# Performance work log

Measured on AMD Instinct MI355X. Metric: run time of the kernel, lower is better.

Reference implementation:

```python
import jax, jax.numpy as jnp
import numpy as np

DIM = 2048
N_HEADS = 16
HEAD_DIM = DIM // N_HEADS
ROPE_BASE = 10000


def l2norm(x, axis=-1, eps=1e-12):
    n = jnp.sqrt(jnp.sum(x * x, axis=axis, keepdims=True))
    return x / jnp.maximum(n, eps)


def rope_tables(T, dim, base, dtype):
    theta = 1.0 / (base ** (jnp.arange(0, dim, 2, dtype=dtype) / dim))  # [dim/2]
    ang = jnp.arange(T, dtype=dtype)[:, None] * theta[None, :]          # [T, dim/2]
    return jnp.sin(ang), jnp.cos(ang)


def apply_rope(x, sin, cos):
    # x: [B, H, T, D]; sin/cos: [T, D/2] (half-split convention, not interleaved)
    half = x.shape[-1] // 2
    xr, xi = x[..., :half], x[..., half:]
    yr = xr * cos - xi * sin
    yi = xr * sin + xi * cos
    return jnp.concatenate([yr, yi], axis=-1)


def setup_inputs() -> dict:
    key = jax.random.key(0)
    ks = jax.random.split(key, 5)
    B, T = 1, 2048
    x = jax.random.normal(ks[0], (B, T, DIM), dtype=jnp.float32)
    wq = jax.random.normal(ks[1], (DIM, DIM), dtype=jnp.float32) * 0.02
    wk = jax.random.normal(ks[2], (DIM, DIM), dtype=jnp.float32) * 0.02
    wv = jax.random.normal(ks[3], (DIM, DIM), dtype=jnp.float32) * 0.02
    wo = jax.random.normal(ks[4], (DIM, DIM), dtype=jnp.float32) * 0.02
    sqk = jnp.ones((N_HEADS, 1, HEAD_DIM), dtype=jnp.float32) * (1.0 / DIM ** 0.5)
    return {"x": x, "wq": wq, "wk": wk, "wv": wv, "wo": wo, "sqk": sqk}


def reference(x, wq, wk, wv, wo, sqk):
    B, T, C = x.shape
    H, D = N_HEADS, HEAD_DIM
    restore = C ** 0.5  # restore_scale_sqk = sqkinit / sqkscale
    actual_sqk = sqk * restore  # [H, 1, D]

    def proj(w):
        return jnp.einsum('btc,oc->bto', x, w).reshape(B, T, H, D).transpose(0, 2, 1, 3)

    q = proj(wq)  # [B, H, T, D]
    new_k = proj(wk)
    new_v = proj(wv)

    sin, cos = rope_tables(T, D, ROPE_BASE, x.dtype)
    q = apply_rope(q, sin, cos) * actual_sqk
    k = apply_rope(new_k, sin, cos) * actual_sqk

    # NOTE: original uses scale=head_dim**0.5 (multiplies by sqrt(D))
    scores = jnp.einsum('bhqd,bhkd->bhqk', q, k) * (D ** 0.5)
    mask = jnp.tril(jnp.ones((T, T), dtype=bool))
    scores = jnp.where(mask, scores, jnp.finfo(scores.dtype).min)
    attn = jax.nn.softmax(scores, axis=-1)
    out = jnp.einsum('bhqk,bhkd->bhqd', attn, new_v)  # [B, H, T, D]
    out = out.transpose(0, 2, 1, 3).reshape(B, T, C)
    out = jnp.einsum('btc,oc->bto', out, wo)
    return (l2norm(out), (new_k, new_v))
```

## Files before the change

kernel.cpp:

```cpp
#include <hip/hip_runtime.h>

typedef __bf16 bf16x8 __attribute__((ext_vector_type(8)));
typedef float f32x4 __attribute__((ext_vector_type(4)));
typedef unsigned short us4 __attribute__((ext_vector_type(4)));

constexpr int TT = 2048;
constexpr int CC = 2048;
constexpr int HH = 16;
constexpr int DD = 128;

__device__ __forceinline__ unsigned short f2bf(float f) {
  unsigned u = __builtin_bit_cast(unsigned, f);
  u += 0x7FFFu + ((u >> 16) & 1u);
  return (unsigned short)(u >> 16);
}
__device__ __forceinline__ float bf2f(unsigned short b) {
  unsigned u = ((unsigned)b) << 16;
  return __builtin_bit_cast(float, u);
}

__device__ __forceinline__ void gld_lds16(const unsigned short* g, unsigned short* l) {
  __builtin_amdgcn_global_load_lds(
      (const __attribute__((address_space(1))) unsigned int*)g,
      (__attribute__((address_space(3))) unsigned int*)l,
      16, 0, 0);
}

__global__ __launch_bounds__(256) void k_cvt5(
    const float* __restrict__ s0, const float* __restrict__ s1,
    const float* __restrict__ s2, const float* __restrict__ s3,
    const float* __restrict__ s4,
    unsigned short* __restrict__ d0, unsigned short* __restrict__ d1,
    unsigned short* __restrict__ d2, unsigned short* __restrict__ d3,
    unsigned short* __restrict__ d4) {
  const int m = blockIdx.y;
  const float* src = (m == 0) ? s0 : (m == 1) ? s1 : (m == 2) ? s2 : (m == 3) ? s3 : s4;
  unsigned short* dst = (m == 0) ? d0 : (m == 1) ? d1 : (m == 2) ? d2 : (m == 3) ? d3 : d4;
  int i = blockIdx.x * 256 + threadIdx.x;
  const float4* s = (const float4*)src;
  float4 a = s[2 * i], b = s[2 * i + 1];
  us4 lo = { f2bf(a.x), f2bf(a.y), f2bf(a.z), f2bf(a.w) };
  us4 hi = { f2bf(b.x), f2bf(b.y), f2bf(b.z), f2bf(b.w) };
  us4* d = (us4*)dst;
  d[2 * i] = lo;
  d[2 * i + 1] = hi;
}

#define WAIT_LGKM0                                      \
  asm volatile("s_waitcnt lgkmcnt(0)" ::: "memory");    \
  __builtin_amdgcn_sched_barrier(0);
#define BAR __builtin_amdgcn_s_barrier();

__global__ __launch_bounds__(512, 2) void k_gemm192(
    const unsigned short* __restrict__ A, const unsigned short* __restrict__ B,
    unsigned short* __restrict__ qraw,
    float* __restrict__ outk, float* __restrict__ outv,
    unsigned short* __restrict__ vtb) {
  __shared__ alignas(16) unsigned short As[2][256 * 64];
  __shared__ alignas(16) unsigned short Bs[2][192 * 64];
  const int K = CC, NT = K >> 6, NT2 = NT >> 1;
  const int tid = threadIdx.x;
  const int m0 = blockIdx.y * 256, n0 = blockIdx.x * 192;
  const int wid = tid >> 6, lane = tid & 63;
  const int wr = wid >> 2, wc = wid & 3;
  const int lr = lane & 15, lg = lane >> 4;

  auto stA = [&](int buf, int jb, int tile) {
#pragma unroll
    for (int j = jb; j < jb + 2; ++j) {
      const int ch = tid + j * 512;
      const int r = ch >> 3, c8 = ch & 7;
      gld_lds16(A + (size_t)(m0 + r) * K + tile * 64 + ((c8 ^ (r & 7)) * 8),
                &As[buf][ch * 8]);
    }
  };
  auto stB2 = [&](int buf, int tile) {
#pragma unroll
    for (int j = 0; j < 2; ++j) {
      const int ch = tid + j * 512;
      const int r = ch >> 3, c8 = ch & 7;
      gld_lds16(B + (size_t)(n0 + r) * K + tile * 64 + ((c8 ^ (r & 7)) * 8),
                &Bs[buf][ch * 8]);
    }
  };
  auto stB1 = [&](int buf, int tile) {
    const int ch = tid + 1024;
    const int r = ch >> 3, c8 = ch & 7;
    gld_lds16(B + (size_t)(n0 + r) * K + tile * 64 + ((c8 ^ (r & 7)) * 8),
              &Bs[buf][ch * 8]);
  };

  f32x4 acc[8][3] = {};
  bf16x8 alo[4][2], ahi[4][2], b01[2][2], b2v[2];

  auto rdAlo = [&](int d) {
#pragma unroll
    for (int im = 0; im < 4; ++im)
#pragma unroll
      for (int kk = 0; kk < 2; ++kk) {
        const int row = wr * 128 + im * 16 + lr;
        alo[im][kk] = *(const bf16x8*)(&As[d][row * 64 + (((kk * 4 + lg) ^ (row & 7)) * 8)]);
      }
  };
  auto rdAhi = [&](int d) {
#pragma unroll
    for (int im = 0; im < 4; ++im)
#pragma unroll
      for (int kk = 0; kk < 2; ++kk) {
        const int row = wr * 128 + (4 + im) * 16 + lr;
        ahi[im][kk] = *(const bf16x8*)(&As[d][row * 64 + (((kk * 4 + lg) ^ (row & 7)) * 8)]);
      }
  };
  auto rdB01 = [&](int d) {
#pragma unroll
    for (int in = 0; in < 2; ++in)
#pragma unroll
      for (int kk = 0; kk < 2; ++kk) {
        const int row = wc * 48 + in * 16 + lr;
        b01[in][kk] = *(const bf16x8*)(&Bs[d][row * 64 + (((kk * 4 + lg) ^ (row & 7)) * 8)]);
      }
  };
  auto rdB2 = [&](int d) {
#pragma unroll
    for (int kk = 0; kk < 2; ++kk) {
      const int row = wc * 48 + 32 + lr;
      b2v[kk] = *(const bf16x8*)(&Bs[d][row * 64 + (((kk * 4 + lg) ^ (row & 7)) * 8)]);
    }
  };

  auto q_lo01 = [&]() {
    __builtin_amdgcn_s_setprio(1);
#pragma unroll
    for (int im = 0; im < 4; ++im)
#pragma unroll
      for (int in = 0; in < 2; ++in)
#pragma unroll
        for (int kk = 0; kk < 2; ++kk)
          acc[im][in] = __builtin_amdgcn_mfma_f32_16x16x32_bf16(alo[im][kk], b01[in][kk], acc[im][in], 0, 0, 0);
    __builtin_amdgcn_s_setprio(0);
  };
  auto q_mid16 = [&]() {
    __builtin_amdgcn_s_setprio(1);
#pragma unroll
    for (int im = 0; im < 4; ++im)
#pragma unroll
      for (int kk = 0; kk < 2; ++kk)
        acc[im][2] = __builtin_amdgcn_mfma_f32_16x16x32_bf16(alo[im][kk], b2v[kk], acc[im][2], 0, 0, 0);
#pragma unroll
    for (int im = 0; im < 4; ++im)
#pragma unroll
      for (int kk = 0; kk < 2; ++kk)
        acc[4 + im][2] = __builtin_amdgcn_mfma_f32_16x16x32_bf16(ahi[im][kk], b2v[kk], acc[4 + im][2], 0, 0, 0);
    __builtin_amdgcn_s_setprio(0);
  };
  auto q_hi01 = [&]() {
    __builtin_amdgcn_s_setprio(1);
#pragma unroll
    for (int im = 0; im < 4; ++im)
#pragma unroll
      for (int in = 0; in < 2; ++in)
#pragma unroll
        for (int kk = 0; kk < 2; ++kk)
          acc[4 + im][in] = __builtin_amdgcn_mfma_f32_16x16x32_bf16(ahi[im][kk], b01[in][kk], acc[4 + im][in], 0, 0, 0);
    __builtin_amdgcn_s_setprio(0);
  };

  stB2(0, 0); stB1(0, 0); stA(0, 0, 0); stA(0, 2, 0);
  stB2(1, 1); stB1(1, 1);
  asm volatile("s_waitcnt vmcnt(3)" ::: "memory");
  __builtin_amdgcn_sched_barrier(0);
  BAR

  for (int t = 0; t < NT2; ++t) {
    const int t1 = 2 * t + 1, t2 = 2 * t + 2, t3 = 2 * t + 3;
    const bool s2 = t2 < NT;

    rdAlo(0); rdB01(0);
    stA(1, 0, t1);
    BAR WAIT_LGKM0
    q_lo01();
    BAR
    rdB2(0); rdAhi(0);
    stA(1, 2, t1);
    BAR WAIT_LGKM0
    q_mid16();
    BAR
    if (s2) { stB2(0, t2); stB1(0, t2); }
    q_hi01();
    if (s2) { asm volatile("s_waitcnt vmcnt(3)" ::: "memory"); }
    else    { asm volatile("s_waitcnt vmcnt(0)" ::: "memory"); }
    __builtin_amdgcn_sched_barrier(0);
    BAR

    rdAlo(1); rdB01(1);
    if (s2) stA(0, 0, t2);
    BAR WAIT_LGKM0
    q_lo01();
    BAR
    rdB2(1); rdAhi(1);
    if (s2) stA(0, 2, t2);
    BAR WAIT_LGKM0
    q_mid16();
    BAR
    if (s2) { stB2(1, t3); stB1(1, t3); }
    q_hi01();
    if (s2) { asm volatile("s_waitcnt vmcnt(3)" ::: "memory"); }
    else    { asm volatile("s_waitcnt vmcnt(0)" ::: "memory"); }
    __builtin_amdgcn_sched_barrier(0);
    BAR
  }

#pragma unroll
  for (int mf = 0; mf < 8; ++mf) {
    const int row = m0 + wr * 128 + mf * 16 + lg * 4;
#pragma unroll
    for (int nf = 0; nf < 3; ++nf) {
      const int col = n0 + wc * 48 + nf * 16 + lr;
      if (col < 2048) {
#pragma unroll
        for (int r = 0; r < 4; ++r)
          qraw[(size_t)(row + r) * 2048 + col] = f2bf(acc[mf][nf][r]);
      } else if (col < 4096) {
        const int c = col - 2048;
#pragma unroll
        for (int r = 0; r < 4; ++r)
          outk[(size_t)(c >> 7) * (TT * DD) + (size_t)(row + r) * DD + (c & 127)] = acc[mf][nf][r];
      } else {
        const int c = col - 4096;
        const int hh = c >> 7, d2 = c & 127;
        us4 tv;
#pragma unroll
        for (int r = 0; r < 4; ++r) {
          float v = acc[mf][nf][r];
          outv[(size_t)hh * (TT * DD) + (size_t)(row + r) * DD + d2] = v;
          tv[r] = f2bf(v);
        }
        *(us4*)(vtb + (size_t)hh * (size_t)(DD * TT) + (size_t)d2 * TT + row) = tv;
      }
    }
  }
}

__global__ __launch_bounds__(512, 2) void k_gemm8p(
    const unsigned short* __restrict__ A, const unsigned short* __restrict__ B,
    int N, int K, int kspan,
    unsigned short* __restrict__ out0, unsigned short* __restrict__ out1,
    unsigned short* __restrict__ out2, unsigned short* __restrict__ out3) {
  __shared__ alignas(16) unsigned short As[2][2][128 * 64];
  __shared__ alignas(16) unsigned short Bs[2][2][128 * 64];
  const int tid = threadIdx.x;
  const int m0 = blockIdx.y * 256, n0 = blockIdx.x * 256;
  const int kbeg = blockIdx.z * kspan;
  const int NT = kspan >> 6, NT2 = NT >> 1;
  const int wid = tid >> 6, lane = tid & 63;
  const int wr = wid >> 2, wc = wid & 3;
  const int lr = lane & 15, lg = lane >> 4;
  const int bh = wc >> 1, brow0 = (wc & 1) * 64;

  const int sr0 = tid >> 3, sc0 = tid & 7;
  const unsigned short* Ab = A + kbeg;
  const unsigned short* Bb = B + kbeg;

  auto stageA = [&](int buf, int half, int tile) {
    const int koff = tile * 64;
#pragma unroll
    for (int j = 0; j < 2; ++j) {
      const int r = sr0 + j * 64;
      gld_lds16(Ab + (size_t)(m0 + half * 128 + r) * K + koff + ((sc0 ^ (r & 7)) * 8),
                &As[buf][half][(tid + j * 512) * 8]);
    }
  };
  auto stageB = [&](int buf, int half, int tile) {
    const int koff = tile * 64;
#pragma unroll
    for (int j = 0; j < 2; ++j) {
      const int r = sr0 + j * 64;
      gld_lds16(Bb + (size_t)(n0 + half * 128 + r) * K + koff + ((sc0 ^ (r & 7)) * 8),
                &Bs[buf][half][(tid + j * 512) * 8]);
    }
  };

  f32x4 acc[8][4] = {};
  bf16x8 alo[4][2], ahi[4][2], ba[2][2], bb[2][2];

  auto rdAlo = [&](int d) {
#pragma unroll
    for (int im = 0; im < 4; ++im)
#pragma unroll
      for (int kk = 0; kk < 2; ++kk) {
        const int row = im * 16 + lr;
        alo[im][kk] = *(const bf16x8*)(&As[d][wr][row * 64 + (((kk * 4 + lg) ^ (row & 7)) * 8)]);
      }
  };
  auto rdAhi = [&](int d) {
#pragma unroll
    for (int im = 0; im < 4; ++im)
#pragma unroll
      for (int kk = 0; kk < 2; ++kk) {
        const int row = (4 + im) * 16 + lr;
        ahi[im][kk] = *(const bf16x8*)(&As[d][wr][row * 64 + (((kk * 4 + lg) ^ (row & 7)) * 8)]);
      }
  };
  auto rdBa = [&](int d) {
#pragma unroll
    for (int in = 0; in < 2; ++in)
#pragma unroll
      for (int kk = 0; kk < 2; ++kk) {
        const int row = brow0 + in * 16 + lr;
        ba[in][kk] = *(const bf16x8*)(&Bs[d][bh][row * 64 + (((kk * 4 + lg) ^ (row & 7)) * 8)]);
      }
  };
  auto rdBb = [&](int d) {
#pragma unroll
    for (int in = 0; in < 2; ++in)
#pragma unroll
      for (int kk = 0; kk < 2; ++kk) {
        const int row = brow0 + (2 + in) * 16 + lr;
        bb[in][kk] = *(const bf16x8*)(&Bs[d][bh][row * 64 + (((kk * 4 + lg) ^ (row & 7)) * 8)]);
      }
  };

#define MFMA_Q(MB, NB, AF, BF)                                                     \
  _Pragma("unroll") for (int im = 0; im < 4; ++im)                                 \
      _Pragma("unroll") for (int in = 0; in < 2; ++in)                             \
          _Pragma("unroll") for (int kk = 0; kk < 2; ++kk)                         \
              acc[MB + im][NB + in] = __builtin_amdgcn_mfma_f32_16x16x32_bf16(     \
                  AF[im][kk], BF[in][kk], acc[MB + im][NB + in], 0, 0, 0);

  stageB(0, 0, 0); stageB(0, 1, 0); stageA(0, 0, 0); stageA(0, 1, 0);
  if (NT > 1) { stageB(1, 0, 1); stageB(1, 1, 1); }
  asm volatile("s_waitcnt vmcnt(4)" ::: "memory");
  __builtin_amdgcn_sched_barrier(0);
  BAR

  for (int t = 0; t < NT2; ++t) {
    const int t1 = 2 * t + 1, t2 = 2 * t + 2, t3 = 2 * t + 3;
    const bool s2 = t2 < NT, s3 = t3 < NT;

    rdAlo(0); rdBa(0); rdBb(0);
    stageA(1, 0, t1); stageA(1, 1, t1);
    BAR WAIT_LGKM0
    __builtin_amdgcn_s_setprio(1);
    MFMA_Q(0, 0, alo, ba)
    MFMA_Q(0, 2, alo, bb)
    __builtin_amdgcn_s_setprio(0);
    BAR
    rdAhi(0);
    if (s2) stageB(0, 0, t2);
    BAR WAIT_LGKM0
    __builtin_amdgcn_s_setprio(1);
    MFMA_Q(4, 2, ahi, bb)
    __builtin_amdgcn_s_setprio(0);
    BAR
    if (s2) stageB(0, 1, t2);
    __builtin_amdgcn_s_setprio(1);
    MFMA_Q(4, 0, ahi, ba)
    __builtin_amdgcn_s_setprio(0);
    if (s2) { asm volatile("s_waitcnt vmcnt(4)" ::: "memory"); }
    else    { asm volatile("s_waitcnt vmcnt(0)" ::: "memory"); }
    __builtin_amdgcn_sched_barrier(0);
    BAR

    rdAlo(1); rdBa(1); rdBb(1);
    if (s2) { stageA(0, 0, t2); stageA(0, 1, t2); }
    BAR WAIT_LGKM0
    __builtin_amdgcn_s_setprio(1);
    MFMA_Q(0, 0, alo, ba)
    MFMA_Q(0, 2, alo, bb)
    __builtin_amdgcn_s_setprio(0);
    BAR
    rdAhi(1);
    if (s3) stageB(1, 0, t3);
    BAR WAIT_LGKM0
    __builtin_amdgcn_s_setprio(1);
    MFMA_Q(4, 2, ahi, bb)
    __builtin_amdgcn_s_setprio(0);
    BAR
    if (s3) stageB(1, 1, t3);
    __builtin_amdgcn_s_setprio(1);
    MFMA_Q(4, 0, ahi, ba)
    __builtin_amdgcn_s_setprio(0);
    if (s3) { asm volatile("s_waitcnt vmcnt(4)" ::: "memory"); }
    else    { asm volatile("s_waitcnt vmcnt(0)" ::: "memory"); }
    __builtin_amdgcn_sched_barrier(0);
    BAR
  }
#undef MFMA_Q

  int z = blockIdx.z;
  unsigned short* dst = (z == 0) ? out0 : (z == 1) ? out1 : (z == 2) ? out2 : out3;
#pragma unroll
  for (int mf = 0; mf < 8; ++mf) {
    const int row = m0 + wr * 128 + mf * 16 + lg * 4;
#pragma unroll
    for (int nf = 0; nf < 4; ++nf) {
      const int col = n0 + wc * 64 + nf * 16 + lr;
#pragma unroll
      for (int r = 0; r < 4; ++r) {
        dst[(size_t)(row + r) * N + col] = f2bf(acc[mf][nf][r]);
      }
    }
  }
}
#undef WAIT_LGKM0
#undef BAR

__global__ __launch_bounds__(256) void k_rope(
    const unsigned short* __restrict__ qraw, const float* __restrict__ Kraw,
    const float* __restrict__ sqk,
    unsigned short* __restrict__ qb, unsigned short* __restrict__ kb) {
  const int t = blockIdx.x;
  __shared__ float sn_s[64], cs_s[64];
  if (threadIdx.x < 64) {
    float theta = expf(-(float)threadIdx.x * 0.14391156831212787f);
    float sn, cs;
    sincosf((float)t * theta, &sn, &cs);
    sn_s[threadIdx.x] = sn;
    cs_s[threadIdx.x] = cs;
  }
  __syncthreads();
  for (int i = threadIdx.x; i < HH * 64; i += 256) {
    int h = i >> 6, dp = i & 63;
    float sn = sn_s[dp], cs = cs_s[dp];
    float qr = bf2f(qraw[(size_t)t * CC + h * DD + dp]);
    float qi = bf2f(qraw[(size_t)t * CC + h * DD + dp + 64]);
    const float* kp = Kraw + (size_t)h * TT * DD + (size_t)t * DD;
    float kr = kp[dp], ki = kp[dp + 64];
    float sr = sqk[h * DD + dp];
    float si = sqk[h * DD + dp + 64];
    float qsr = sr * 512.0f, qsi = si * 512.0f;
    float ksr = sr * 45.25483399593904f, ksi = si * 45.25483399593904f;
    unsigned short* qo = qb + ((size_t)h * TT + t) * DD;
    unsigned short* ko = kb + ((size_t)h * TT + t) * DD;
    qo[dp]      = f2bf((qr * cs - qi * sn) * qsr);
    qo[dp + 64] = f2bf((qr * sn + qi * cs) * qsi);
    ko[dp]      = f2bf((kr * cs - ki * sn) * ksr);
    ko[dp + 64] = f2bf((kr * sn + ki * cs) * ksi);
  }
}

__global__ __launch_bounds__(256, 2) void k_attn(
    const unsigned short* __restrict__ qb, const unsigned short* __restrict__ kb,
    const unsigned short* __restrict__ vt, unsigned short* __restrict__ ob) {
  const int h = blockIdx.x;
  const int gy = blockIdx.y;
  const int gA = (gy < 16) ? gy : 47 - gy;
  const int ntiles = gA + 1;
  const int tid = threadIdx.x;
  const int wid = tid >> 6, lane = tid & 63;
  const int lr = lane & 15, lg = lane >> 4;
  const int q0 = gA * 64 + wid * 16;

  __shared__ alignas(16) unsigned short Ks[2][64 * 128];
  __shared__ alignas(16) unsigned short Vs[2][128 * 64];
  __shared__ alignas(16) unsigned short P[4][16][72];

  const unsigned short* qh = qb + (size_t)h * TT * DD;
  const unsigned short* kh = kb + (size_t)h * TT * DD;
  const unsigned short* vh = vt + (size_t)h * DD * TT;

  auto stageKV = [&](int buf, int kt) {
    const int k0 = kt * 64;
#pragma unroll
    for (int j = 0; j < 4; ++j) {
      int ch = tid + j * 256;
      int r = ch >> 4, c4 = ch & 15;
      gld_lds16(kh + (size_t)(k0 + r) * DD + ((c4 ^ (r & 7)) * 8), Ks[buf] + ch * 8);
    }
#pragma unroll
    for (int j = 0; j < 4; ++j) {
      int ch = tid + j * 256;
      int d = ch >> 3, c8 = ch & 7;
      gld_lds16(vh + (size_t)d * TT + k0 + ((c8 ^ (d & 7)) * 8), Vs[buf] + ch * 8);
    }
  };

  bf16x8 qf[4];
#pragma unroll
  for (int c = 0; c < 4; ++c)
    qf[c] = *(const bf16x8*)(qh + (size_t)(q0 + lr) * DD + c * 32 + lg * 8);

  f32x4 acc[8] = {};
  float mrow[4] = {-3e38f, -3e38f, -3e38f, -3e38f};
  float lsum[4] = {0.f, 0.f, 0.f, 0.f};

  stageKV(0, 0);
  asm volatile("s_waitcnt vmcnt(0)" ::: "memory");
  __builtin_amdgcn_sched_barrier(0);
  __builtin_amdgcn_s_barrier();

  for (int kt = 0; kt < ntiles; ++kt) {
    const int cur = kt & 1;
    const int k0 = kt * 64;
    const bool pf = (kt + 1) < ntiles;
    if (pf) stageKV(cur ^ 1, kt + 1);

    {
      f32x4 sv[4] = {};
#pragma unroll
      for (int ktile = 0; ktile < 4; ++ktile) {
        const int row = ktile * 16 + lr;
#pragma unroll
        for (int c = 0; c < 4; ++c) {
          int chn = (c * 4 + lg) ^ (lr & 7);
          bf16x8 kf = *(const bf16x8*)(Ks[cur] + row * 128 + chn * 8);
          sv[ktile] = __builtin_amdgcn_mfma_f32_16x16x32_bf16(qf[c], kf, sv[ktile], 0, 0, 0);
        }
      }
      if (k0 + 63 > q0) {
#pragma unroll
        for (int ktile = 0; ktile < 4; ++ktile)
#pragma unroll
          for (int r = 0; r < 4; ++r) {
            int key = k0 + ktile * 16 + lr;
            int qrow = q0 + lg * 4 + r;
            if (key > qrow) sv[ktile][r] = -1e30f;
          }
      }
      float pmax[4];
#pragma unroll
      for (int r = 0; r < 4; ++r)
        pmax[r] = fmaxf(fmaxf(sv[0][r], sv[1][r]), fmaxf(sv[2][r], sv[3][r]));
#pragma unroll
      for (int msk = 1; msk <= 8; msk <<= 1)
#pragma unroll
        for (int r = 0; r < 4; ++r) pmax[r] = fmaxf(pmax[r], __shfl_xor(pmax[r], msk));
      float p[4][4], ps[4], scl[4];
#pragma unroll
      for (int r = 0; r < 4; ++r) {
        float mn = fmaxf(mrow[r], pmax[r]);
        scl[r] = __expf(mrow[r] - mn);
        mrow[r] = mn;
        ps[r] = 0.f;
#pragma unroll
        for (int ktile = 0; ktile < 4; ++ktile) {
          p[ktile][r] = __expf(sv[ktile][r] - mn);
          ps[r] += p[ktile][r];
        }
      }
#pragma unroll
      for (int msk = 1; msk <= 8; msk <<= 1)
#pragma unroll
        for (int r = 0; r < 4; ++r) ps[r] += __shfl_xor(ps[r], msk);
#pragma unroll
      for (int r = 0; r < 4; ++r) lsum[r] = lsum[r] * scl[r] + ps[r];
#pragma unroll
      for (int n = 0; n < 8; ++n)
#pragma unroll
        for (int r = 0; r < 4; ++r) acc[n][r] *= scl[r];
#pragma unroll
      for (int ktile = 0; ktile < 4; ++ktile)
#pragma unroll
        for (int r = 0; r < 4; ++r)
          P[wid][lg * 4 + r][ktile * 16 + lr] = f2bf(p[ktile][r]);
      asm volatile("s_waitcnt lgkmcnt(0)" ::: "memory");
      __builtin_amdgcn_sched_barrier(0);
      bf16x8 pf2[2];
#pragma unroll
      for (int ks = 0; ks < 2; ++ks)
        pf2[ks] = *(const bf16x8*)(&P[wid][lr][ks * 32 + lg * 8]);
#pragma unroll
      for (int n = 0; n < 8; ++n) {
        const int row = n * 16 + lr;
#pragma unroll
        for (int ks = 0; ks < 2; ++ks) {
          int chn = (ks * 4 + lg) ^ (lr & 7);
          bf16x8 vf = *(const bf16x8*)(Vs[cur] + row * 64 + chn * 8);
          acc[n] = __builtin_amdgcn_mfma_f32_16x16x32_bf16(pf2[ks], vf, acc[n], 0, 0, 0);
        }
      }
    }
    if (pf) {
      asm volatile("s_waitcnt vmcnt(0)" ::: "memory");
      __builtin_amdgcn_sched_barrier(0);
      __builtin_amdgcn_s_barrier();
    }
  }

  float inv[4];
#pragma unroll
  for (int r = 0; r < 4; ++r) inv[r] = 1.0f / lsum[r];
#pragma unroll
  for (int n = 0; n < 8; ++n)
#pragma unroll
    for (int r = 0; r < 4; ++r) {
      int t = q0 + lg * 4 + r;
      ob[(size_t)t * CC + h * DD + n * 16 + lr] = f2bf(acc[n][r] * inv[r]);
    }
}

__global__ __launch_bounds__(256) void k_l2norm(
    const unsigned short* __restrict__ Of0, const unsigned short* __restrict__ Of1,
    const unsigned short* __restrict__ Of2, const unsigned short* __restrict__ Of3,
    float* __restrict__ out) {
  const int t = blockIdx.x;
  const int tid = threadIdx.x;
  const size_t base = (size_t)t * CC + tid * 8;
  bf16x8 a0 = *(const bf16x8*)(Of0 + base);
  bf16x8 a1 = *(const bf16x8*)(Of1 + base);
  bf16x8 a2 = *(const bf16x8*)(Of2 + base);
  bf16x8 a3 = *(const bf16x8*)(Of3 + base);
  float v[8];
  float ss = 0.f;
#pragma unroll
  for (int j = 0; j < 8; ++j) {
    v[j] = (float)a0[j] + (float)a1[j] + (float)a2[j] + (float)a3[j];
    ss += v[j] * v[j];
  }
#pragma unroll
  for (int msk = 1; msk < 64; msk <<= 1) ss += __shfl_xor(ss, msk);
  __shared__ float red[4];
  if ((tid & 63) == 0) red[tid >> 6] = ss;
  __syncthreads();
  ss = red[0] + red[1] + red[2] + red[3];
  float sc = 1.0f / fmaxf(sqrtf(ss), 1e-12f);
  float4 oa = { v[0] * sc, v[1] * sc, v[2] * sc, v[3] * sc };
  float4 obv = { v[4] * sc, v[5] * sc, v[6] * sc, v[7] * sc };
  float4* o = (float4*)(out + base);
  o[0] = oa;
  o[1] = obv;
}

extern "C" void kernel_launch(void* const* d_in, const int* in_sizes, int n_in,
                              void* d_out, int out_size, void* d_ws, size_t ws_size,
                              hipStream_t stream) {
  const float* x   = (const float*)d_in[0];
  const float* wq  = (const float*)d_in[1];
  const float* wk  = (const float*)d_in[2];
  const float* wv  = (const float*)d_in[3];
  const float* wo  = (const float*)d_in[4];
  const float* sqk = (const float*)d_in[5];

  float* out_norm = (float*)d_out;
  float* out_k = out_norm + (size_t)4 * 1024 * 1024;
  float* out_v = out_norm + (size_t)8 * 1024 * 1024;

  char* ws = (char*)d_ws;
  unsigned short* xb  = (unsigned short*)(ws);
  unsigned short* w1b = (unsigned short*)(ws + (8u << 20));
  unsigned short* wob = (unsigned short*)(ws + (32u << 20));
  unsigned short* qb  = (unsigned short*)(ws + (40u << 20));
  unsigned short* kb  = (unsigned short*)(ws + (48u << 20));
  unsigned short* vtb = (unsigned short*)(ws + (56u << 20));
  unsigned short* obb = (unsigned short*)(ws + (64u << 20));
  unsigned short* qraw = (unsigned short*)(ws + (72u << 20));

  unsigned short* Of0 = (unsigned short*)(ws + (72u << 20));
  unsigned short* Of1 = (unsigned short*)(ws);
  unsigned short* Of2 = (unsigned short*)(ws + (8u << 20));
  unsigned short* Of3 = (unsigned short*)(ws + (16u << 20));

  k_cvt5<<<dim3(2048, 5), 256, 0, stream>>>(
      x, wq, wk, wv, wo,
      xb, w1b, w1b + (size_t)4 * 1024 * 1024, w1b + (size_t)8 * 1024 * 1024, wob);

  k_gemm192<<<dim3(32, 8), 512, 0, stream>>>(xb, w1b, qraw, out_k, out_v, vtb);

  k_rope<<<TT, 256, 0, stream>>>(qraw, out_k, sqk, qb, kb);

  k_attn<<<dim3(16, 32), 256, 0, stream>>>(qb, kb, vtb, obb);

  k_gemm8p<<<dim3(8, 8, 4), 512, 0, stream>>>(obb, wob, CC, CC, CC / 4,
                                              Of0, Of1, Of2, Of3);

  k_l2norm<<<TT, 256, 0, stream>>>(Of0, Of1, Of2, Of3, out_norm);
}
```

Measured before the change: 182.6 us.

## Replace split-K 256x256 output GEMM with full-K 128x128 tile GEMM

The output projection GEMM moves from a split-K kernel (256x256 tiles, K split four ways into four bf16 partial buffers) to a full-K kernel with 128x128 tiles and 256 threads, launched on a 16x16 grid. It uses a simpler double-buffered loop with one barrier per k-tile. The l2norm kernel now reads one output buffer instead of summing four partials. This removes the partial-sum traffic and the bf16 rounding of each partial, at the cost of smaller tiles with less reuse and a longer K loop per block.

```diff
diff --git a/kernel.cpp b/kernel.cpp
--- a/kernel.cpp
+++ b/kernel.cpp
@@ -241,164 +241,116 @@
   }
 }
 
-__global__ __launch_bounds__(512, 2) void k_gemm8p(
+__global__ __launch_bounds__(256, 2) void k_gemm128(
     const unsigned short* __restrict__ A, const unsigned short* __restrict__ B,
-    int N, int K, int kspan,
-    unsigned short* __restrict__ out0, unsigned short* __restrict__ out1,
-    unsigned short* __restrict__ out2, unsigned short* __restrict__ out3) {
-  __shared__ alignas(16) unsigned short As[2][2][128 * 64];
-  __shared__ alignas(16) unsigned short Bs[2][2][128 * 64];
+    int N, int K, unsigned short* __restrict__ out0) {
+  __shared__ alignas(16) unsigned short As[2][128 * 64];
+  __shared__ alignas(16) unsigned short Bs[2][128 * 64];
   const int tid = threadIdx.x;
-  const int m0 = blockIdx.y * 256, n0 = blockIdx.x * 256;
-  const int kbeg = blockIdx.z * kspan;
-  const int NT = kspan >> 6, NT2 = NT >> 1;
+  const int m0 = blockIdx.y * 128, n0 = blockIdx.x * 128;
+  const int NT = K >> 6;
   const int wid = tid >> 6, lane = tid & 63;
-  const int wr = wid >> 2, wc = wid & 3;
+  const int wr = wid >> 1, wc = wid & 1;
   const int lr = lane & 15, lg = lane >> 4;
-  const int bh = wc >> 1, brow0 = (wc & 1) * 64;
-
-  const int sr0 = tid >> 3, sc0 = tid & 7;
-  const unsigned short* Ab = A + kbeg;
-  const unsigned short* Bb = B + kbeg;
-
-  auto stageA = [&](int buf, int half, int tile) {
-    const int koff = tile * 64;
-#pragma unroll
-    for (int j = 0; j < 2; ++j) {
-      const int r = sr0 + j * 64;
-      gld_lds16(Ab + (size_t)(m0 + half * 128 + r) * K + koff + ((sc0 ^ (r & 7)) * 8),
-                &As[buf][half][(tid + j * 512) * 8]);
-    }
-  };
-  auto stageB = [&](int buf, int half, int tile) {
-    const int koff = tile * 64;
-#pragma unroll
-    for (int j = 0; j < 2; ++j) {
-      const int r = sr0 + j * 64;
-      gld_lds16(Bb + (size_t)(n0 + half * 128 + r) * K + koff + ((sc0 ^ (r & 7)) * 8),
-                &Bs[buf][half][(tid + j * 512) * 8]);
-    }
-  };
-
-  f32x4 acc[8][4] = {};
-  bf16x8 alo[4][2], ahi[4][2], ba[2][2], bb[2][2];
-
-  auto rdAlo = [&](int d) {
-#pragma unroll
-    for (int im = 0; im < 4; ++im)
+
+  auto stageA = [&](int buf, int koff) {
+#pragma unroll
+    for (int j = 0; j < 4; ++j) {
+      const int ch = tid + j * 256;
+      const int r = ch >> 3, c8 = ch & 7;
+      gld_lds16(A + (size_t)(m0 + r) * K + koff + ((c8 ^ (r & 7)) * 8),
+                &As[buf][ch * 8]);
+    }
+  };
+  auto stageB = [&](int buf, int koff) {
+#pragma unroll
+    for (int j = 0; j < 4; ++j) {
+      const int ch = tid + j * 256;
+      const int r = ch >> 3, c8 = ch & 7;
+      gld_lds16(B + (size_t)(n0 + r) * K + koff + ((c8 ^ (r & 7)) * 8),
+                &Bs[buf][ch * 8]);
+    }
+  };
+
+  f32x4 acc[4][4] = {};
+
+  stageA(0, 0); stageB(0, 0);
+  stageA(1, 64); stageB(1, 64);
+  asm volatile("s_waitcnt vmcnt(8)" ::: "memory");
+  __builtin_amdgcn_sched_barrier(0);
+  __builtin_amdgcn_s_barrier();
+
+  for (int t = 0; t < NT; ++t) {
+    const int cur = t & 1;
+    bf16x8 av[4][2], b01[2][2], b23[2][2];
+
+#pragma unroll
+    for (int m = 0; m < 4; ++m)
 #pragma unroll
       for (int kk = 0; kk < 2; ++kk) {
-        const int row = im * 16 + lr;
-        alo[im][kk] = *(const bf16x8*)(&As[d][wr][row * 64 + (((kk * 4 + lg) ^ (row & 7)) * 8)]);
-      }
-  };
-  auto rdAhi = [&](int d) {
-#pragma unroll
-    for (int im = 0; im < 4; ++im)
+        const int row = wr * 64 + m * 16 + lr;
+        av[m][kk] = *(const bf16x8*)(&As[cur][row * 64 + (((kk * 4 + lg) ^ (row & 7)) * 8)]);
+      }
+#pragma unroll
+    for (int n = 0; n < 2; ++n)
 #pragma unroll
       for (int kk = 0; kk < 2; ++kk) {
-        const int row = (4 + im) * 16 + lr;
-        ahi[im][kk] = *(const bf16x8*)(&As[d][wr][row * 64 + (((kk * 4 + lg) ^ (row & 7)) * 8)]);
-      }
-  };
-  auto rdBa = [&](int d) {
-#pragma unroll
-    for (int in = 0; in < 2; ++in)
+        const int row = wc * 64 + n * 16 + lr;
+        b01[n][kk] = *(const bf16x8*)(&Bs[cur][row * 64 + (((kk * 4 + lg) ^ (row & 7)) * 8)]);
+      }
+#pragma unroll
+    for (int n = 0; n < 2; ++n)
 #pragma unroll
       for (int kk = 0; kk < 2; ++kk) {
-        const int row = brow0 + in * 16 + lr;
-        ba[in][kk] = *(const bf16x8*)(&Bs[d][bh][row * 64 + (((kk * 4 + lg) ^ (row & 7)) * 8)]);
-      }
-  };
-  auto rdBb = [&](int d) {
-#pragma unroll
-    for (int in = 0; in < 2; ++in)
-#pragma unroll
-      for (int kk = 0; kk < 2; ++kk) {
-        const int row = brow0 + (2 + in) * 16 + lr;
-        bb[in][kk] = *(const bf16x8*)(&Bs[d][bh][row * 64 + (((kk * 4 + lg) ^ (row & 7)) * 8)]);
-      }
-  };
-
-#define MFMA_Q(MB, NB, AF, BF)                                                     \
-  _Pragma("unroll") for (int im = 0; im < 4; ++im)                                 \
-      _Pragma("unroll") for (int in = 0; in < 2; ++in)                             \
-          _Pragma("unroll") for (int kk = 0; kk < 2; ++kk)                         \
-              acc[MB + im][NB + in] = __builtin_amdgcn_mfma_f32_16x16x32_bf16(     \
-                  AF[im][kk], BF[in][kk], acc[MB + im][NB + in], 0, 0, 0);
-
-  stageB(0, 0, 0); stageB(0, 1, 0); stageA(0, 0, 0); stageA(0, 1, 0);
-  if (NT > 1) { stageB(1, 0, 1); stageB(1, 1, 1); }
-  asm volatile("s_waitcnt vmcnt(4)" ::: "memory");
-  __builtin_amdgcn_sched_barrier(0);
-  BAR
-
-  for (int t = 0; t < NT2; ++t) {
-    const int t1 = 2 * t + 1, t2 = 2 * t + 2, t3 = 2 * t + 3;
-    const bool s2 = t2 < NT, s3 = t3 < NT;
-
-    rdAlo(0); rdBa(0); rdBb(0);
-    stageA(1, 0, t1); stageA(1, 1, t1);
-    BAR WAIT_LGKM0
+        const int row = wc * 64 + (2 + n) * 16 + lr;
+        b23[n][kk] = *(const bf16x8*)(&Bs[cur][row * 64 + (((kk * 4 + lg) ^ (row & 7)) * 8)]);
+      }
+    asm volatile("s_waitcnt lgkmcnt(4)" ::: "memory");
+    __builtin_amdgcn_sched_barrier(0);
+
     __builtin_amdgcn_s_setprio(1);
-    MFMA_Q(0, 0, alo, ba)
-    MFMA_Q(0, 2, alo, bb)
+#pragma unroll
+    for (int m = 0; m < 4; ++m)
+#pragma unroll
+      for (int n = 0; n < 2; ++n)
+#pragma unroll
+        for (int kk = 0; kk < 2; ++kk)
+          acc[m][n] = __builtin_amdgcn_mfma_f32_16x16x32_bf16(av[m][kk], b01[n][kk], acc[m][n], 0, 0, 0);
     __builtin_amdgcn_s_setprio(0);
-    BAR
-    rdAhi(0);
-    if (s2) stageB(0, 0, t2);
-    BAR WAIT_LGKM0
+    asm volatile("s_waitcnt lgkmcnt(0)" ::: "memory");
+    __builtin_amdgcn_sched_barrier(0);
+
     __builtin_amdgcn_s_setprio(1);
-    MFMA_Q(4, 2, ahi, bb)
+#pragma unroll
+    for (int m = 0; m < 4; ++m)
+#pragma unroll
+      for (int n = 0; n < 2; ++n)
+#pragma unroll
+        for (int kk = 0; kk < 2; ++kk)
+          acc[m][2 + n] = __builtin_amdgcn_mfma_f32_16x16x32_bf16(av[m][kk], b23[n][kk], acc[m][2 + n], 0, 0, 0);
     __builtin_amdgcn_s_setprio(0);
-    BAR
-    if (s2) stageB(0, 1, t2);
-    __builtin_amdgcn_s_setprio(1);
-    MFMA_Q(4, 0, ahi, ba)
-    __builtin_amdgcn_s_setprio(0);
-    if (s2) { asm volatile("s_waitcnt vmcnt(4)" ::: "memory"); }
-    else    { asm volatile("s_waitcnt vmcnt(0)" ::: "memory"); }
     __builtin_amdgcn_sched_barrier(0);
-    BAR
-
-    rdAlo(1); rdBa(1); rdBb(1);
-    if (s2) { stageA(0, 0, t2); stageA(0, 1, t2); }
-    BAR WAIT_LGKM0
-    __builtin_amdgcn_s_setprio(1);
-    MFMA_Q(0, 0, alo, ba)
-    MFMA_Q(0, 2, alo, bb)
-    __builtin_amdgcn_s_setprio(0);
-    BAR
-    rdAhi(1);
-    if (s3) stageB(1, 0, t3);
-    BAR WAIT_LGKM0
-    __builtin_amdgcn_s_setprio(1);
-    MFMA_Q(4, 2, ahi, bb)
-    __builtin_amdgcn_s_setprio(0);
-    BAR
-    if (s3) stageB(1, 1, t3);
-    __builtin_amdgcn_s_setprio(1);
-    MFMA_Q(4, 0, ahi, ba)
-    __builtin_amdgcn_s_setprio(0);
-    if (s3) { asm volatile("s_waitcnt vmcnt(4)" ::: "memory"); }
-    else    { asm volatile("s_waitcnt vmcnt(0)" ::: "memory"); }
-    __builtin_amdgcn_sched_barrier(0);
-    BAR
-  }
-#undef MFMA_Q
-
-  int z = blockIdx.z;
-  unsigned short* dst = (z == 0) ? out0 : (z == 1) ? out1 : (z == 2) ? out2 : out3;
-#pragma unroll
-  for (int mf = 0; mf < 8; ++mf) {
-    const int row = m0 + wr * 128 + mf * 16 + lg * 4;
-#pragma unroll
-    for (int nf = 0; nf < 4; ++nf) {
-      const int col = n0 + wc * 64 + nf * 16 + lr;
-#pragma unroll
-      for (int r = 0; r < 4; ++r) {
-        dst[(size_t)(row + r) * N + col] = f2bf(acc[mf][nf][r]);
-      }
+
+    __builtin_amdgcn_s_barrier();
+    if (t + 2 < NT) {
+      stageA(cur, (t + 2) * 64); stageB(cur, (t + 2) * 64);
+      asm volatile("s_waitcnt vmcnt(8)" ::: "memory");
+      __builtin_amdgcn_sched_barrier(0);
+    } else if (t + 1 < NT) {
+      asm volatile("s_waitcnt vmcnt(0)" ::: "memory");
+      __builtin_amdgcn_sched_barrier(0);
+    }
+  }
+
+#pragma unroll
+  for (int m = 0; m < 4; ++m) {
+    const int row = m0 + wr * 64 + m * 16 + lg * 4;
+#pragma unroll
+    for (int n = 0; n < 4; ++n) {
+      const int col = n0 + wc * 64 + n * 16 + lr;
+#pragma unroll
+      for (int r = 0; r < 4; ++r)
+        out0[(size_t)(row + r) * N + col] = f2bf(acc[m][n][r]);
     }
   }
 }
@@ -590,21 +542,16 @@
 }
 
 __global__ __launch_bounds__(256) void k_l2norm(
-    const unsigned short* __restrict__ Of0, const unsigned short* __restrict__ Of1,
-    const unsigned short* __restrict__ Of2, const unsigned short* __restrict__ Of3,
-    float* __restrict__ out) {
+    const unsigned short* __restrict__ Of, float* __restrict__ out) {
   const int t = blockIdx.x;
   const int tid = threadIdx.x;
   const size_t base = (size_t)t * CC + tid * 8;
-  bf16x8 a0 = *(const bf16x8*)(Of0 + base);
-  bf16x8 a1 = *(const bf16x8*)(Of1 + base);
-  bf16x8 a2 = *(const bf16x8*)(Of2 + base);
-  bf16x8 a3 = *(const bf16x8*)(Of3 + base);
+  bf16x8 a0 = *(const bf16x8*)(Of + base);
   float v[8];
   float ss = 0.f;
 #pragma unroll
   for (int j = 0; j < 8; ++j) {
-    v[j] = (float)a0[j] + (float)a1[j] + (float)a2[j] + (float)a3[j];
+    v[j] = (float)a0[j];
     ss += v[j] * v[j];
   }
 #pragma unroll
@@ -645,10 +592,7 @@
   unsigned short* obb = (unsigned short*)(ws + (64u << 20));
   unsigned short* qraw = (unsigned short*)(ws + (72u << 20));
 
-  unsigned short* Of0 = (unsigned short*)(ws + (72u << 20));
-  unsigned short* Of1 = (unsigned short*)(ws);
-  unsigned short* Of2 = (unsigned short*)(ws + (8u << 20));
-  unsigned short* Of3 = (unsigned short*)(ws + (16u << 20));
+  unsigned short* OfO = (unsigned short*)(ws + (72u << 20));
 
   k_cvt5<<<dim3(2048, 5), 256, 0, stream>>>(
       x, wq, wk, wv, wo,
@@ -660,8 +604,7 @@
 
   k_attn<<<dim3(16, 32), 256, 0, stream>>>(qb, kb, vtb, obb);
 
-  k_gemm8p<<<dim3(8, 8, 4), 512, 0, stream>>>(obb, wob, CC, CC, CC / 4,
-                                              Of0, Of1, Of2, Of3);
-
-  k_l2norm<<<TT, 256, 0, stream>>>(Of0, Of1, Of2, Of3, out_norm);
-}
+  k_gemm128<<<dim3(16, 16), 256, 0, stream>>>(obb, wob, CC, CC, OfO);
+
+  k_l2norm<<<TT, 256, 0, stream>>>(OfO, out_norm);
+}
```

Measured after the change: 190.0 us. 4.0% more time.
